# Performance work log

Measured on AMD Instinct MI355X. Metric: run time of the kernel, lower is better.

## Reference

```python
import jax, jax.numpy as jnp
import numpy as np

NUM_HEADS = 8
WINDOW = 128  # num_previous_frames
EPS = 1e-5


def setup_inputs() -> dict:
    key = jax.random.key(0)
    ks = jax.random.split(key, 5)
    B, T, E = 8, 1024, 512
    x = jax.random.normal(ks[0], (B, T, E), dtype=jnp.float32)
    x_lengths = jax.random.randint(ks[1], (B,), 1, T + 1).astype(jnp.int32)
    gamma = jnp.ones((E,), dtype=jnp.float32)
    beta = jnp.zeros((E,), dtype=jnp.float32)
    sc_in = 1.0 / np.sqrt(E)
    w_in = jax.random.normal(ks[2], (3 * E, E), dtype=jnp.float32) * sc_in
    b_in = jnp.zeros((3 * E,), dtype=jnp.float32)
    w_out = jax.random.normal(ks[3], (E, E), dtype=jnp.float32) * sc_in
    b_out = jnp.zeros((E,), dtype=jnp.float32)
    return {"x": x, "x_lengths": x_lengths, "gamma": gamma, "beta": beta,
            "w_in": w_in, "b_in": b_in, "w_out": w_out, "b_out": b_out}


def _forward(x, gamma, beta, w_in, b_in, w_out, b_out):
    B, T, E = x.shape
    H = NUM_HEADS
    D = E // H
    # Timewise LayerNorm: normalize over channel dim per (batch, time)
    mu = jnp.mean(x, axis=-1, keepdims=True)
    var = jnp.mean(jnp.square(x - mu), axis=-1, keepdims=True)
    xn = (x - mu) * jax.lax.rsqrt(var + EPS) * gamma + beta
    # in-projection: qkv packed
    qkv = xn @ w_in.T + b_in  # [B,T,3E]
    q, k, v = jnp.split(qkv, 3, axis=-1)
    q = q.reshape(B, T, H, D)
    k = k.reshape(B, T, H, D)
    v = v.reshape(B, T, H, D)
    scale = 1.0 / np.sqrt(D)
    scores = jnp.einsum('bqhd,bkhd->bhqk', q * scale, k)  # [B,H,T,T]
    # banded causal mask: allow j in [i-WINDOW, i]
    i = jnp.arange(T)[:, None]
    j = jnp.arange(T)[None, :]
    allowed = (j <= i) & (j >= i - WINDOW)
    scores = jnp.where(allowed[None, None], scores, -jnp.inf)
    attn = jax.nn.softmax(scores, axis=-1)
    ctx = jnp.einsum('bhqk,bkhd->bqhd', attn, v).reshape(B, T, E)
    out = ctx @ w_out.T + b_out
    return out  # dropout is identity in eval mode


def reference(x, x_lengths, gamma, beta, w_in, b_in, w_out, b_out):
    del x_lengths  # unused by the original forward (no key_padding_mask passed)
    return _forward(x, gamma, beta, w_in, b_in, w_out, b_out)
```

## Files before the change

### kernel.cpp

```cpp
#include <hip/hip_runtime.h>
#include <stdint.h>

typedef __bf16 bf16;
typedef __bf16 bf16x8 __attribute__((ext_vector_type(8)));
typedef float f32x4 __attribute__((ext_vector_type(4)));

#define MFMA_16x16x32(a, b, c) __builtin_amdgcn_mfma_f32_16x16x32_bf16((a), (b), (c), 0, 0, 0)

__device__ __forceinline__ void gl_lds16(const bf16* g, bf16* l) {
    __builtin_amdgcn_global_load_lds(
        (const __attribute__((address_space(1))) void*)g,
        (__attribute__((address_space(3))) void*)l, 16, 0, 0);
}

__global__ __launch_bounds__(256) void prep_kernel(const float* __restrict__ x,
                                                   const float* __restrict__ gamma,
                                                   const float* __restrict__ beta,
                                                   const float* __restrict__ w_in,
                                                   const float* __restrict__ w_out,
                                                   bf16* __restrict__ xn,
                                                   bf16* __restrict__ cw_in,
                                                   bf16* __restrict__ cw_out) {
    const int bid = blockIdx.x;
    if (bid < 2048) {
        const int lane = threadIdx.x & 63;
        const int row = (bid << 2) + (threadIdx.x >> 6);
        const size_t base = (size_t)row * 512 + lane * 8;
        const float* xf = x + base;
        float4 a = *(const float4*)xf;
        float4 b = *(const float4*)(xf + 4);
        float f[8] = {a.x, a.y, a.z, a.w, b.x, b.y, b.z, b.w};
        float s = 0.f;
#pragma unroll
        for (int j = 0; j < 8; ++j) s += f[j];
#pragma unroll
        for (int off = 32; off >= 1; off >>= 1) s += __shfl_xor(s, off, 64);
        const float mu = s * (1.0f / 512.0f);
        float vs = 0.f;
#pragma unroll
        for (int j = 0; j < 8; ++j) { float d = f[j] - mu; vs += d * d; }
#pragma unroll
        for (int off = 32; off >= 1; off >>= 1) vs += __shfl_xor(vs, off, 64);
        const float rstd = rsqrtf(vs * (1.0f / 512.0f) + 1e-5f);
        float4 g0 = *(const float4*)(gamma + lane * 8);
        float4 g1 = *(const float4*)(gamma + lane * 8 + 4);
        float4 b0 = *(const float4*)(beta + lane * 8);
        float4 b1 = *(const float4*)(beta + lane * 8 + 4);
        float gg[8] = {g0.x, g0.y, g0.z, g0.w, g1.x, g1.y, g1.z, g1.w};
        float bb[8] = {b0.x, b0.y, b0.z, b0.w, b1.x, b1.y, b1.z, b1.w};
        bf16x8 o;
#pragma unroll
        for (int j = 0; j < 8; ++j)
            o[j] = (bf16)((f[j] - mu) * rstd * gg[j] + bb[j]);
        *(bf16x8*)(xn + base) = o;
    } else {
        const float* src;
        bf16* dst;
        int base;
        if (bid < 2432) { src = w_in;  dst = cw_in;  base = (bid - 2048) * 2048; }
        else            { src = w_out; dst = cw_out; base = (bid - 2432) * 2048; }
        const int i = base + threadIdx.x * 8;
        float4 a = *(const float4*)(src + i);
        float4 b = *(const float4*)(src + i + 4);
        float f[8] = {a.x, a.y, a.z, a.w, b.x, b.y, b.z, b.w};
        bf16x8 o;
#pragma unroll
        for (int j = 0; j < 8; ++j) o[j] = (bf16)f[j];
        *(bf16x8*)(dst + i) = o;
    }
}

template <int TM, typename OT>
__global__ __launch_bounds__(256) void gemm_bt(const bf16* __restrict__ A,
                                               const bf16* __restrict__ B,
                                               const float* __restrict__ bias,
                                               OT* __restrict__ C,
                                               int N, int K) {
    constexpr int MI = TM / 32;
    constexpr int NCA = TM * 8;
    __shared__ alignas(16) bf16 As[TM * 64];
    __shared__ alignas(16) bf16 Bs[128 * 64];
    const int tid = threadIdx.x;
    const int lane = tid & 63;
    const int wid = tid >> 6;
    const int wm = (wid >> 1) * (TM / 2), wn = (wid & 1) * 64;
    const int m0 = blockIdx.y * TM, n0 = blockIdx.x * 128;
    const int l15 = lane & 15, l16 = lane >> 4;

    f32x4 acc[MI][4] = {};

    const bf16* Abase = A + (size_t)m0 * K;
    const bf16* Bbase = B + (size_t)n0 * K;

    for (int k0 = 0; k0 < K; k0 += 64) {
#pragma unroll
        for (int c = tid; c < NCA; c += 256) {
            const int p = c / (TM * 4);
            const int r = (c % (TM * 4)) >> 2;
            const int ko = (c & 3) * 8 + p * 32;
            gl_lds16(Abase + (size_t)r * K + k0 + ko, &As[c * 8]);
        }
#pragma unroll
        for (int c = tid; c < 1024; c += 256) {
            const int p = c >> 9;
            const int r = (c & 511) >> 2;
            const int ko = (c & 3) * 8 + p * 32;
            gl_lds16(Bbase + (size_t)r * K + k0 + ko, &Bs[c * 8]);
        }
        __syncthreads();
#pragma unroll
        for (int h = 0; h < 2; ++h) {
            bf16x8 af[MI], bfr[4];
#pragma unroll
            for (int t = 0; t < MI; ++t)
                af[t] = *(const bf16x8*)&As[h * (TM * 32) + (wm + t * 16 + l15) * 32 + l16 * 8];
#pragma unroll
            for (int t = 0; t < 4; ++t)
                bfr[t] = *(const bf16x8*)&Bs[h * 4096 + (wn + t * 16 + l15) * 32 + l16 * 8];
#pragma unroll
            for (int i = 0; i < MI; ++i)
#pragma unroll
                for (int j = 0; j < 4; ++j)
                    acc[i][j] = MFMA_16x16x32(af[i], bfr[j], acc[i][j]);
        }
        __syncthreads();
    }

#pragma unroll
    for (int j = 0; j < 4; ++j) {
        const int col = n0 + wn + j * 16 + l15;
        const float bv = bias[col];
#pragma unroll
        for (int i = 0; i < MI; ++i) {
            const int rbase = m0 + wm + i * 16 + l16 * 4;
#pragma unroll
            for (int r = 0; r < 4; ++r)
                C[(size_t)(rbase + r) * N + col] = (OT)(acc[i][j][r] + bv);
        }
    }
}

#define KS_STRIDE 72
#define VN_STRIDE 74
#define PW_STRIDE 40

__global__ __launch_bounds__(256) void attn_kernel(const bf16* __restrict__ qkv,
                                                   bf16* __restrict__ ctx) {
    __shared__ alignas(16) bf16 Ks[192 * KS_STRIDE];
    __shared__ alignas(16) bf16 Vn[192 * VN_STRIDE];
    __shared__ alignas(16) bf16 Pbuf[4 * 16 * PW_STRIDE];

    const int tid = threadIdx.x;
    const int lane = tid & 63, wid = tid >> 6;
    const int l15 = lane & 15, l16 = lane >> 4;
    const int bh = blockIdx.y, b = bh >> 3, h = bh & 7;
    const int q0 = blockIdx.x * 64;
    const int kv0 = (q0 > 128) ? (q0 - 128) : 0;
    const int nk = q0 + 64 - kv0;
    const size_t tokbase = (size_t)b * 1024;

    for (int c = tid; c < nk * 8; c += 256) {
        const int kk = c >> 3, dc = (c & 7) * 8;
        const bf16* src = qkv + (tokbase + kv0 + kk) * 1536 + h * 64 + dc;
        uint4 kw = *(const uint4*)(src + 512);
        *(uint4*)&Ks[kk * KS_STRIDE + dc] = kw;
        uint4 vw = *(const uint4*)(src + 1024);
        uint* vdst = (uint*)&Vn[kk * VN_STRIDE + dc];
        vdst[0] = vw.x; vdst[1] = vw.y; vdst[2] = vw.z; vdst[3] = vw.w;
    }

    const int qt0 = q0 + wid * 16;
    const bf16* qptr = qkv + (tokbase + qt0 + l15) * 1536 + h * 64;
    bf16x8 qa0 = *(const bf16x8*)(qptr + l16 * 8);
    bf16x8 qa1 = *(const bf16x8*)(qptr + 32 + l16 * 8);

    __syncthreads();

    bf16* Pw = &Pbuf[wid * 16 * PW_STRIDE];
    f32x4 of[4] = {};
    float mst[4], lst[4];
#pragma unroll
    for (int r = 0; r < 4; ++r) { mst[r] = -1e30f; lst[r] = 0.f; }

    const int ktstart = ((qt0 > 128) ? (qt0 - 128) : 0) & ~31;
    for (int kt = ktstart; kt <= qt0 + 15; kt += 32) {
        const int krel = kt - kv0;
        f32x4 s0 = {}, s1 = {};
        {
            const bf16* kb0 = &Ks[(krel + l15) * KS_STRIDE + l16 * 8];
            const bf16* kb1 = kb0 + 16 * KS_STRIDE;
            s0 = MFMA_16x16x32(qa0, *(const bf16x8*)kb0, s0);
            s0 = MFMA_16x16x32(qa1, *(const bf16x8*)(kb0 + 32), s0);
            s1 = MFMA_16x16x32(qa0, *(const bf16x8*)kb1, s1);
            s1 = MFMA_16x16x32(qa1, *(const bf16x8*)(kb1 + 32), s1);
        }
        float e0[4], e1[4];
#pragma unroll
        for (int r = 0; r < 4; ++r) {
            const int qa = qt0 + l16 * 4 + r;
            const int kg0 = kt + l15;
            const int kg1 = kg0 + 16;
            const bool ok0 = (kg0 <= qa) && (kg0 >= qa - 128);
            const bool ok1 = (kg1 <= qa) && (kg1 >= qa - 128);
            float v0 = ok0 ? s0[r] * 0.125f : -1e30f;
            float v1 = ok1 ? s1[r] * 0.125f : -1e30f;
            float mx = fmaxf(v0, v1);
#pragma unroll
            for (int off = 1; off < 16; off <<= 1)
                mx = fmaxf(mx, __shfl_xor(mx, off, 64));
            const float mnew = fmaxf(mst[r], mx);
            const float alpha = __expf(mst[r] - mnew);
            e0[r] = ok0 ? __expf(v0 - mnew) : 0.f;
            e1[r] = ok1 ? __expf(v1 - mnew) : 0.f;
            float rs = e0[r] + e1[r];
#pragma unroll
            for (int off = 1; off < 16; off <<= 1)
                rs += __shfl_xor(rs, off, 64);
            lst[r] = lst[r] * alpha + rs;
            mst[r] = mnew;
#pragma unroll
            for (int nt = 0; nt < 4; ++nt) of[nt][r] *= alpha;
        }
#pragma unroll
        for (int r = 0; r < 4; ++r) {
            const int q = l16 * 4 + r;
            Pw[q * PW_STRIDE + l15] = (bf16)e0[r];
            Pw[q * PW_STRIDE + 16 + l15] = (bf16)e1[r];
        }
        __asm__ volatile("s_waitcnt lgkmcnt(0)" ::: "memory");
        bf16x8 pa = *(const bf16x8*)&Pw[l15 * PW_STRIDE + l16 * 8];
        int row[8];
#pragma unroll
        for (int j = 0; j < 8; ++j) {
            int rr = krel + l16 * 8 + j;
            row[j] = (rr < nk) ? rr : (nk - 1);
        }
#pragma unroll
        for (int nt = 0; nt < 4; ++nt) {
            bf16x8 vb;
#pragma unroll
            for (int j = 0; j < 8; ++j)
                vb[j] = Vn[row[j] * VN_STRIDE + nt * 16 + l15];
            of[nt] = MFMA_16x16x32(pa, vb, of[nt]);
        }
        __asm__ volatile("s_waitcnt lgkmcnt(0)" ::: "memory");
    }

    float linv[4];
#pragma unroll
    for (int r = 0; r < 4; ++r) linv[r] = 1.0f / lst[r];
    bf16* cbase = ctx + (tokbase + qt0) * 512 + h * 64;
#pragma unroll
    for (int nt = 0; nt < 4; ++nt)
#pragma unroll
        for (int r = 0; r < 4; ++r) {
            const int q = l16 * 4 + r;
            cbase[(size_t)q * 512 + nt * 16 + l15] = (bf16)(of[nt][r] * linv[r]);
        }
}

extern "C" void kernel_launch(void* const* d_in, const int* in_sizes, int n_in,
                              void* d_out, int out_size, void* d_ws, size_t ws_size,
                              hipStream_t stream) {
    const float* x     = (const float*)d_in[0];
    const float* gamma = (const float*)d_in[2];
    const float* beta  = (const float*)d_in[3];
    const float* w_in  = (const float*)d_in[4];
    const float* b_in  = (const float*)d_in[5];
    const float* w_out = (const float*)d_in[6];
    const float* b_out = (const float*)d_in[7];
    float* out = (float*)d_out;

    char* ws = (char*)d_ws;
    bf16* cw_in  = (bf16*)ws;
    bf16* cw_out = cw_in + 786432;
    bf16* xn     = (bf16*)(ws + (4u << 20));
    bf16* qkv    = (bf16*)(ws + (12u << 20));
    bf16* ctx    = xn;

    prep_kernel<<<2560, 256, 0, stream>>>(x, gamma, beta, w_in, w_out, xn, cw_in, cw_out);
    gemm_bt<128, bf16><<<dim3(12, 64), 256, 0, stream>>>(xn, cw_in, b_in, qkv, 1536, 512);
    attn_kernel<<<dim3(16, 64), 256, 0, stream>>>(qkv, ctx);
    gemm_bt<64, float><<<dim3(4, 128), 256, 0, stream>>>(ctx, cw_out, b_out, out, 512, 512);
}
```

Measured before the change: 138.3 us.

## Fuse all stages into one cooperative persistent kernel with grid syncs

Replaces the four separate launches (prep, QKV GEMM, attention, out GEMM) with one cooperative mega-kernel of 512 blocks that runs each stage in a loop over work units and separates stages with grid.sync. GEMM tiles change to 128x96 and 128x64 so the unit counts divide evenly, and attention now streams K/V through shared memory in 64-row chunks to cut LDS use for two-blocks-per-CU occupancy. The aim is to remove launch gaps and tail effects between kernels. The cost is grid-barrier overhead, fixed work per block, and extra syncthreads in attention. A fallback to separate launches is kept in case the cooperative launch fails.

```diff
diff --git a/kernel.cpp b/kernel.cpp
--- a/kernel.cpp
+++ b/kernel.cpp
@@ -1,5 +1,8 @@
 #include <hip/hip_runtime.h>
+#include <hip/hip_cooperative_groups.h>
 #include <stdint.h>
+
+namespace cg = cooperative_groups;
 
 typedef __bf16 bf16;
 typedef __bf16 bf16x8 __attribute__((ext_vector_type(8)));
@@ -13,18 +16,18 @@
         (__attribute__((address_space(3))) void*)l, 16, 0, 0);
 }
 
-__global__ __launch_bounds__(256) void prep_kernel(const float* __restrict__ x,
-                                                   const float* __restrict__ gamma,
-                                                   const float* __restrict__ beta,
-                                                   const float* __restrict__ w_in,
-                                                   const float* __restrict__ w_out,
-                                                   bf16* __restrict__ xn,
-                                                   bf16* __restrict__ cw_in,
-                                                   bf16* __restrict__ cw_out) {
-    const int bid = blockIdx.x;
-    if (bid < 2048) {
-        const int lane = threadIdx.x & 63;
-        const int row = (bid << 2) + (threadIdx.x >> 6);
+__device__ __forceinline__ void prep_unit(int u, const float* __restrict__ x,
+                                          const float* __restrict__ gamma,
+                                          const float* __restrict__ beta,
+                                          const float* __restrict__ w_in,
+                                          const float* __restrict__ w_out,
+                                          bf16* __restrict__ xn,
+                                          bf16* __restrict__ cw_in,
+                                          bf16* __restrict__ cw_out) {
+    const int tid = threadIdx.x;
+    if (u < 2048) {
+        const int lane = tid & 63;
+        const int row = (u << 2) + (tid >> 6);
         const size_t base = (size_t)row * 512 + lane * 8;
         const float* xf = x + base;
         float4 a = *(const float4*)xf;
@@ -57,9 +60,9 @@
         const float* src;
         bf16* dst;
         int base;
-        if (bid < 2432) { src = w_in;  dst = cw_in;  base = (bid - 2048) * 2048; }
-        else            { src = w_out; dst = cw_out; base = (bid - 2432) * 2048; }
-        const int i = base + threadIdx.x * 8;
+        if (u < 2432) { src = w_in;  dst = cw_in;  base = (u - 2048) * 2048; }
+        else          { src = w_out; dst = cw_out; base = (u - 2432) * 2048; }
+        const int i = base + tid * 8;
         float4 a = *(const float4*)(src + i);
         float4 b = *(const float4*)(src + i + 4);
         float f[8] = {a.x, a.y, a.z, a.w, b.x, b.y, b.z, b.w};
@@ -70,64 +73,63 @@
     }
 }
 
-template <int TM, typename OT>
-__global__ __launch_bounds__(256) void gemm_bt(const bf16* __restrict__ A,
-                                               const bf16* __restrict__ B,
-                                               const float* __restrict__ bias,
-                                               OT* __restrict__ C,
-                                               int N, int K) {
-    constexpr int MI = TM / 32;
-    constexpr int NCA = TM * 8;
-    __shared__ alignas(16) bf16 As[TM * 64];
-    __shared__ alignas(16) bf16 Bs[128 * 64];
+template <int TM, int TN, typename OT>
+__device__ __forceinline__ void gemm_tile(const bf16* __restrict__ A,
+                                          const bf16* __restrict__ B,
+                                          const float* __restrict__ bias,
+                                          OT* __restrict__ C,
+                                          int N, int K, int m0, int n0,
+                                          char* smem) {
+    constexpr int MI = TM / 32, NI = TN / 32;
+    bf16* As = (bf16*)smem;
+    bf16* Bs = (bf16*)(smem + TM * 128);
     const int tid = threadIdx.x;
     const int lane = tid & 63;
     const int wid = tid >> 6;
-    const int wm = (wid >> 1) * (TM / 2), wn = (wid & 1) * 64;
-    const int m0 = blockIdx.y * TM, n0 = blockIdx.x * 128;
+    const int wm = (wid >> 1) * (TM / 2), wn = (wid & 1) * (TN / 2);
     const int l15 = lane & 15, l16 = lane >> 4;
 
-    f32x4 acc[MI][4] = {};
+    f32x4 acc[MI][NI] = {};
 
     const bf16* Abase = A + (size_t)m0 * K;
     const bf16* Bbase = B + (size_t)n0 * K;
 
     for (int k0 = 0; k0 < K; k0 += 64) {
 #pragma unroll
-        for (int c = tid; c < NCA; c += 256) {
+        for (int c = tid; c < TM * 8; c += 256) {
             const int p = c / (TM * 4);
             const int r = (c % (TM * 4)) >> 2;
             const int ko = (c & 3) * 8 + p * 32;
             gl_lds16(Abase + (size_t)r * K + k0 + ko, &As[c * 8]);
         }
 #pragma unroll
-        for (int c = tid; c < 1024; c += 256) {
-            const int p = c >> 9;
-            const int r = (c & 511) >> 2;
+        for (int c = tid; c < TN * 8; c += 256) {
+            const int p = c / (TN * 4);
+            const int r = (c % (TN * 4)) >> 2;
             const int ko = (c & 3) * 8 + p * 32;
             gl_lds16(Bbase + (size_t)r * K + k0 + ko, &Bs[c * 8]);
         }
         __syncthreads();
 #pragma unroll
         for (int h = 0; h < 2; ++h) {
-            bf16x8 af[MI], bfr[4];
+            bf16x8 af[MI], bfr[NI];
 #pragma unroll
             for (int t = 0; t < MI; ++t)
                 af[t] = *(const bf16x8*)&As[h * (TM * 32) + (wm + t * 16 + l15) * 32 + l16 * 8];
 #pragma unroll
-            for (int t = 0; t < 4; ++t)
-                bfr[t] = *(const bf16x8*)&Bs[h * 4096 + (wn + t * 16 + l15) * 32 + l16 * 8];
+            for (int t = 0; t < NI; ++t)
+                bfr[t] = *(const bf16x8*)&Bs[h * (TN * 32) + (wn + t * 16 + l15) * 32 + l16 * 8];
 #pragma unroll
             for (int i = 0; i < MI; ++i)
 #pragma unroll
-                for (int j = 0; j < 4; ++j)
+                for (int j = 0; j < NI; ++j)
                     acc[i][j] = MFMA_16x16x32(af[i], bfr[j], acc[i][j]);
         }
         __syncthreads();
     }
 
 #pragma unroll
-    for (int j = 0; j < 4; ++j) {
+    for (int j = 0; j < NI; ++j) {
         const int col = n0 + wn + j * 16 + l15;
         const float bv = bias[col];
 #pragma unroll
@@ -144,38 +146,27 @@
 #define VN_STRIDE 74
 #define PW_STRIDE 40
 
-__global__ __launch_bounds__(256) void attn_kernel(const bf16* __restrict__ qkv,
-                                                   bf16* __restrict__ ctx) {
-    __shared__ alignas(16) bf16 Ks[192 * KS_STRIDE];
-    __shared__ alignas(16) bf16 Vn[192 * VN_STRIDE];
-    __shared__ alignas(16) bf16 Pbuf[4 * 16 * PW_STRIDE];
+__device__ __forceinline__ void attn_unit(int qtile, int bh,
+                                          const bf16* __restrict__ qkv,
+                                          bf16* __restrict__ ctx,
+                                          char* smem) {
+    bf16* Ks   = (bf16*)smem;
+    bf16* Vn   = (bf16*)(smem + 9216);
+    bf16* Pbuf = (bf16*)(smem + 18688);
 
     const int tid = threadIdx.x;
     const int lane = tid & 63, wid = tid >> 6;
     const int l15 = lane & 15, l16 = lane >> 4;
-    const int bh = blockIdx.y, b = bh >> 3, h = bh & 7;
-    const int q0 = blockIdx.x * 64;
+    const int b = bh >> 3, h = bh & 7;
+    const int q0 = qtile * 64;
     const int kv0 = (q0 > 128) ? (q0 - 128) : 0;
-    const int nk = q0 + 64 - kv0;
     const size_t tokbase = (size_t)b * 1024;
-
-    for (int c = tid; c < nk * 8; c += 256) {
-        const int kk = c >> 3, dc = (c & 7) * 8;
-        const bf16* src = qkv + (tokbase + kv0 + kk) * 1536 + h * 64 + dc;
-        uint4 kw = *(const uint4*)(src + 512);
-        *(uint4*)&Ks[kk * KS_STRIDE + dc] = kw;
-        uint4 vw = *(const uint4*)(src + 1024);
-        uint* vdst = (uint*)&Vn[kk * VN_STRIDE + dc];
-        vdst[0] = vw.x; vdst[1] = vw.y; vdst[2] = vw.z; vdst[3] = vw.w;
-    }
 
     const int qt0 = q0 + wid * 16;
     const bf16* qptr = qkv + (tokbase + qt0 + l15) * 1536 + h * 64;
     bf16x8 qa0 = *(const bf16x8*)(qptr + l16 * 8);
     bf16x8 qa1 = *(const bf16x8*)(qptr + 32 + l16 * 8);
 
-    __syncthreads();
-
     bf16* Pw = &Pbuf[wid * 16 * PW_STRIDE];
     f32x4 of[4] = {};
     float mst[4], lst[4];
@@ -183,67 +174,78 @@
     for (int r = 0; r < 4; ++r) { mst[r] = -1e30f; lst[r] = 0.f; }
 
     const int ktstart = ((qt0 > 128) ? (qt0 - 128) : 0) & ~31;
-    for (int kt = ktstart; kt <= qt0 + 15; kt += 32) {
-        const int krel = kt - kv0;
-        f32x4 s0 = {}, s1 = {};
-        {
-            const bf16* kb0 = &Ks[(krel + l15) * KS_STRIDE + l16 * 8];
-            const bf16* kb1 = kb0 + 16 * KS_STRIDE;
-            s0 = MFMA_16x16x32(qa0, *(const bf16x8*)kb0, s0);
-            s0 = MFMA_16x16x32(qa1, *(const bf16x8*)(kb0 + 32), s0);
-            s1 = MFMA_16x16x32(qa0, *(const bf16x8*)kb1, s1);
-            s1 = MFMA_16x16x32(qa1, *(const bf16x8*)(kb1 + 32), s1);
-        }
-        float e0[4], e1[4];
-#pragma unroll
-        for (int r = 0; r < 4; ++r) {
-            const int qa = qt0 + l16 * 4 + r;
-            const int kg0 = kt + l15;
-            const int kg1 = kg0 + 16;
-            const bool ok0 = (kg0 <= qa) && (kg0 >= qa - 128);
-            const bool ok1 = (kg1 <= qa) && (kg1 >= qa - 128);
-            float v0 = ok0 ? s0[r] * 0.125f : -1e30f;
-            float v1 = ok1 ? s1[r] * 0.125f : -1e30f;
-            float mx = fmaxf(v0, v1);
-#pragma unroll
-            for (int off = 1; off < 16; off <<= 1)
-                mx = fmaxf(mx, __shfl_xor(mx, off, 64));
-            const float mnew = fmaxf(mst[r], mx);
-            const float alpha = __expf(mst[r] - mnew);
-            e0[r] = ok0 ? __expf(v0 - mnew) : 0.f;
-            e1[r] = ok1 ? __expf(v1 - mnew) : 0.f;
-            float rs = e0[r] + e1[r];
-#pragma unroll
-            for (int off = 1; off < 16; off <<= 1)
-                rs += __shfl_xor(rs, off, 64);
-            lst[r] = lst[r] * alpha + rs;
-            mst[r] = mnew;
-#pragma unroll
-            for (int nt = 0; nt < 4; ++nt) of[nt][r] *= alpha;
-        }
-#pragma unroll
-        for (int r = 0; r < 4; ++r) {
-            const int q = l16 * 4 + r;
-            Pw[q * PW_STRIDE + l15] = (bf16)e0[r];
-            Pw[q * PW_STRIDE + 16 + l15] = (bf16)e1[r];
-        }
-        __asm__ volatile("s_waitcnt lgkmcnt(0)" ::: "memory");
-        bf16x8 pa = *(const bf16x8*)&Pw[l15 * PW_STRIDE + l16 * 8];
-        int row[8];
-#pragma unroll
-        for (int j = 0; j < 8; ++j) {
-            int rr = krel + l16 * 8 + j;
-            row[j] = (rr < nk) ? rr : (nk - 1);
-        }
-#pragma unroll
-        for (int nt = 0; nt < 4; ++nt) {
-            bf16x8 vb;
-#pragma unroll
-            for (int j = 0; j < 8; ++j)
-                vb[j] = Vn[row[j] * VN_STRIDE + nt * 16 + l15];
-            of[nt] = MFMA_16x16x32(pa, vb, of[nt]);
-        }
-        __asm__ volatile("s_waitcnt lgkmcnt(0)" ::: "memory");
+    const int ktend = qt0 + 15;
+
+    for (int c0 = kv0; c0 < q0 + 64; c0 += 64) {
+        for (int c = tid; c < 512; c += 256) {
+            const int kk = c >> 3, dc = (c & 7) * 8;
+            const bf16* src = qkv + (tokbase + c0 + kk) * 1536 + h * 64 + dc;
+            *(uint4*)&Ks[kk * KS_STRIDE + dc] = *(const uint4*)(src + 512);
+            uint4 vw = *(const uint4*)(src + 1024);
+            uint* vdst = (uint*)&Vn[kk * VN_STRIDE + dc];
+            vdst[0] = vw.x; vdst[1] = vw.y; vdst[2] = vw.z; vdst[3] = vw.w;
+        }
+        __syncthreads();
+
+        const int klo = (ktstart > c0) ? ktstart : c0;
+        const int khi = (ktend < c0 + 63) ? ktend : c0 + 63;
+        for (int kt = klo; kt <= khi; kt += 32) {
+            const int krel = kt - c0;
+            f32x4 s0 = {}, s1 = {};
+            {
+                const bf16* kb0 = &Ks[(krel + l15) * KS_STRIDE + l16 * 8];
+                const bf16* kb1 = kb0 + 16 * KS_STRIDE;
+                s0 = MFMA_16x16x32(qa0, *(const bf16x8*)kb0, s0);
+                s0 = MFMA_16x16x32(qa1, *(const bf16x8*)(kb0 + 32), s0);
+                s1 = MFMA_16x16x32(qa0, *(const bf16x8*)kb1, s1);
+                s1 = MFMA_16x16x32(qa1, *(const bf16x8*)(kb1 + 32), s1);
+            }
+            float e0[4], e1[4];
+#pragma unroll
+            for (int r = 0; r < 4; ++r) {
+                const int qa = qt0 + l16 * 4 + r;
+                const int kg0 = kt + l15;
+                const int kg1 = kg0 + 16;
+                const bool ok0 = (kg0 <= qa) && (kg0 >= qa - 128);
+                const bool ok1 = (kg1 <= qa) && (kg1 >= qa - 128);
+                float v0 = ok0 ? s0[r] * 0.125f : -1e30f;
+                float v1 = ok1 ? s1[r] * 0.125f : -1e30f;
+                float mx = fmaxf(v0, v1);
+#pragma unroll
+                for (int off = 1; off < 16; off <<= 1)
+                    mx = fmaxf(mx, __shfl_xor(mx, off, 64));
+                const float mnew = fmaxf(mst[r], mx);
+                const float alpha = __expf(mst[r] - mnew);
+                e0[r] = ok0 ? __expf(v0 - mnew) : 0.f;
+                e1[r] = ok1 ? __expf(v1 - mnew) : 0.f;
+                float rs = e0[r] + e1[r];
+#pragma unroll
+                for (int off = 1; off < 16; off <<= 1)
+                    rs += __shfl_xor(rs, off, 64);
+                lst[r] = lst[r] * alpha + rs;
+                mst[r] = mnew;
+#pragma unroll
+                for (int nt = 0; nt < 4; ++nt) of[nt][r] *= alpha;
+            }
+#pragma unroll
+            for (int r = 0; r < 4; ++r) {
+                const int q = l16 * 4 + r;
+                Pw[q * PW_STRIDE + l15] = (bf16)e0[r];
+                Pw[q * PW_STRIDE + 16 + l15] = (bf16)e1[r];
+            }
+            __asm__ volatile("s_waitcnt lgkmcnt(0)" ::: "memory");
+            bf16x8 pa = *(const bf16x8*)&Pw[l15 * PW_STRIDE + l16 * 8];
+#pragma unroll
+            for (int nt = 0; nt < 4; ++nt) {
+                bf16x8 vb;
+#pragma unroll
+                for (int j = 0; j < 8; ++j)
+                    vb[j] = Vn[(krel + l16 * 8 + j) * VN_STRIDE + nt * 16 + l15];
+                of[nt] = MFMA_16x16x32(pa, vb, of[nt]);
+            }
+            __asm__ volatile("s_waitcnt lgkmcnt(0)" ::: "memory");
+        }
+        __syncthreads();
     }
 
     float linv[4];
@@ -257,6 +259,77 @@
             const int q = l16 * 4 + r;
             cbase[(size_t)q * 512 + nt * 16 + l15] = (bf16)(of[nt][r] * linv[r]);
         }
+}
+
+__global__ __launch_bounds__(256, 2) void mega_kernel(const float* __restrict__ x,
+                                                      const float* __restrict__ gamma,
+                                                      const float* __restrict__ beta,
+                                                      const float* __restrict__ w_in,
+                                                      const float* __restrict__ b_in,
+                                                      const float* __restrict__ w_out,
+                                                      const float* __restrict__ b_out,
+                                                      float* __restrict__ out,
+                                                      char* __restrict__ ws) {
+    __shared__ __align__(16) char smem[28672];
+
+    bf16* cw_in  = (bf16*)ws;
+    bf16* cw_out = cw_in + 786432;
+    bf16* xn     = (bf16*)(ws + (4u << 20));
+    bf16* qkv    = (bf16*)(ws + (12u << 20));
+    bf16* ctx    = xn;
+
+    const int bid = blockIdx.x;
+    cg::grid_group grid = cg::this_grid();
+
+#pragma unroll
+    for (int i = 0; i < 5; ++i)
+        prep_unit(bid * 5 + i, x, gamma, beta, w_in, w_out, xn, cw_in, cw_out);
+    __threadfence();
+    grid.sync();
+
+#pragma unroll
+    for (int i = 0; i < 2; ++i) {
+        const int u = bid * 2 + i;
+        gemm_tile<128, 96, bf16>(xn, cw_in, b_in, qkv, 1536, 512,
+                                 (u >> 4) * 128, (u & 15) * 96, smem);
+    }
+    __threadfence();
+    grid.sync();
+
+#pragma unroll
+    for (int i = 0; i < 2; ++i) {
+        const int u = bid * 2 + i;
+        attn_unit(u >> 6, u & 63, qkv, ctx, smem);
+        __syncthreads();
+    }
+    __threadfence();
+    grid.sync();
+
+    gemm_tile<128, 64, float>(ctx, cw_out, b_out, out, 512, 512,
+                              (bid >> 3) * 128, (bid & 7) * 64, smem);
+}
+
+__global__ __launch_bounds__(256) void prep_kernel_fb(const float* x, const float* gamma,
+                                                      const float* beta, const float* w_in,
+                                                      const float* w_out, bf16* xn,
+                                                      bf16* cw_in, bf16* cw_out) {
+    prep_unit(blockIdx.x, x, gamma, beta, w_in, w_out, xn, cw_in, cw_out);
+}
+__global__ __launch_bounds__(256) void gemm_qkv_fb(const bf16* A, const bf16* B,
+                                                   const float* bias, bf16* C) {
+    __shared__ __align__(16) char smem[28672];
+    gemm_tile<128, 96, bf16>(A, B, bias, C, 1536, 512,
+                             (blockIdx.x >> 4) * 128, (blockIdx.x & 15) * 96, smem);
+}
+__global__ __launch_bounds__(256) void attn_fb(const bf16* qkv, bf16* ctx) {
+    __shared__ __align__(16) char smem[23808];
+    attn_unit(blockIdx.x >> 6, blockIdx.x & 63, qkv, ctx, smem);
+}
+__global__ __launch_bounds__(256) void gemm_out_fb(const bf16* A, const bf16* B,
+                                                   const float* bias, float* C) {
+    __shared__ __align__(16) char smem[24576];
+    gemm_tile<128, 64, float>(A, B, bias, C, 512, 512,
+                              (blockIdx.x >> 3) * 128, (blockIdx.x & 7) * 64, smem);
 }
 
 extern "C" void kernel_launch(void* const* d_in, const int* in_sizes, int n_in,
@@ -270,16 +343,23 @@
     const float* w_out = (const float*)d_in[6];
     const float* b_out = (const float*)d_in[7];
     float* out = (float*)d_out;
-
     char* ws = (char*)d_ws;
-    bf16* cw_in  = (bf16*)ws;
-    bf16* cw_out = cw_in + 786432;
-    bf16* xn     = (bf16*)(ws + (4u << 20));
-    bf16* qkv    = (bf16*)(ws + (12u << 20));
-    bf16* ctx    = xn;
-
-    prep_kernel<<<2560, 256, 0, stream>>>(x, gamma, beta, w_in, w_out, xn, cw_in, cw_out);
-    gemm_bt<128, bf16><<<dim3(12, 64), 256, 0, stream>>>(xn, cw_in, b_in, qkv, 1536, 512);
-    attn_kernel<<<dim3(16, 64), 256, 0, stream>>>(qkv, ctx);
-    gemm_bt<64, float><<<dim3(4, 128), 256, 0, stream>>>(ctx, cw_out, b_out, out, 512, 512);
-}
+
+    void* args[] = {(void*)&x, (void*)&gamma, (void*)&beta, (void*)&w_in,
+                    (void*)&b_in, (void*)&w_out, (void*)&b_out, (void*)&out,
+                    (void*)&ws};
+    hipError_t e = hipLaunchCooperativeKernel((void*)mega_kernel, dim3(512),
+                                              dim3(256), args, 0, stream);
+    if (e != hipSuccess) {
+        bf16* cw_in  = (bf16*)ws;
+        bf16* cw_out = cw_in + 786432;
+        bf16* xn     = (bf16*)(ws + (4u << 20));
+        bf16* qkv    = (bf16*)(ws + (12u << 20));
+        bf16* ctx    = xn;
+        prep_kernel_fb<<<2560, 256, 0, stream>>>(x, gamma, beta, w_in, w_out,
+                                                 xn, cw_in, cw_out);
+        gemm_qkv_fb<<<1024, 256, 0, stream>>>(xn, cw_in, b_in, qkv);
+        attn_fb<<<1024, 256, 0, stream>>>(qkv, ctx);
+        gemm_out_fb<<<512, 256, 0, stream>>>(ctx, cw_out, b_out, out);
+    }
+}
```

Measured after the change: 512.8 us. 3.71x slower.
